# Optimization experiments

Measured on AMD Instinct MI355X. Metric: run time of the kernel, lower is better.

The kernel has to match this reference:

```python
import jax, jax.numpy as jnp
import numpy as np

ALPHA = 0.2  # leaky_relu negative slope
NEG_INF = -9e15


def gat_layer(h_in, W, a, adj_mask):
    """One GATLayer (eval mode, dropout disabled).
    h_in: [N, F_in], W: [F_in, F_out], a: [2*F_out, 1], adj_mask: [N, N] bool.
    Equivalent to the torch repeat/cat construction: e_ij = leaky_relu(a1.h_i + a2.h_j).
    """
    h = h_in @ W                          # [N, F_out]
    F_out = W.shape[1]
    a1 = a[:F_out, 0]                     # [F_out]
    a2 = a[F_out:, 0]                     # [F_out]
    f1 = h @ a1                           # [N]
    f2 = h @ a2                           # [N]
    e = jax.nn.leaky_relu(f1[:, None] + f2[None, :], negative_slope=ALPHA)  # [N, N]
    e = jnp.where(adj_mask, e, NEG_INF)
    attn = jax.nn.softmax(e, axis=-1)     # rows sum to 1
    return jax.nn.elu(attn @ h)           # [N, F_out]


def setup_inputs() -> dict:
    key = jax.random.key(0)
    ks = jax.random.split(key, 6)
    N, F_in, F_hid, F_out, H = 8192, 29, 8, 2, 4
    x = jax.random.normal(ks[0], (N, F_in), dtype=jnp.float32)
    adj = jax.random.randint(ks[1], (N, N), 0, 2, dtype=jnp.int32)
    # xavier_uniform with gain=1.414
    def xavier(k, shape, gain=1.414):
        fan_in, fan_out = shape[0], shape[1]
        bound = gain * np.sqrt(6.0 / (fan_in + fan_out))
        return jax.random.uniform(k, shape, jnp.float32, -bound, bound)
    W_heads = jnp.stack([xavier(k, (F_in, F_hid)) for k in jax.random.split(ks[2], H)])   # [H, 29, 8]
    a_heads = jnp.stack([xavier(k, (2 * F_hid, 1)) for k in jax.random.split(ks[3], H)])  # [H, 16, 1]
    W_out = xavier(ks[4], (F_hid * H, F_out))   # [32, 2]
    a_out = xavier(ks[5], (2 * F_out, 1))       # [4, 1]
    return {"x": x, "adj": adj, "W_heads": W_heads, "a_heads": a_heads,
            "W_out": W_out, "a_out": a_out}


def reference(x, adj, W_heads, a_heads, W_out, a_out):
    adj_mask = adj > 0
    heads = jax.vmap(lambda W, a: gat_layer(x, W, a, adj_mask))(W_heads, a_heads)  # [H, N, 8]
    hcat = jnp.concatenate(list(heads), axis=1)   # [N, H*8] (same order as torch cat over heads)
    out = gat_layer(hcat, W_out, a_out, adj_mask)  # [N, 2]
    return jax.nn.log_softmax(out, axis=1)
```

## Files before the change

kernel.cpp:

```cpp
#include <hip/hip_runtime.h>
#include <math.h>

#define N 8192
#define NW 128
#define FIN 29
#define FH 8
#define NH 4
#define ALPHA 0.2f
#define LOG2E 1.4426950408889634f

typedef unsigned long long ull;

__device__ inline unsigned bf16rn(float f) {
    unsigned u = __float_as_uint(f);
    return (u + 0x7fffu + ((u >> 16) & 1u)) >> 16;
}
__device__ inline float2 bfpair(unsigned u) {
    return make_float2(__uint_as_float(u << 16), __uint_as_float(u & 0xffff0000u));
}
__device__ inline unsigned fenc(float x) {
    unsigned u = __float_as_uint(x);
    return (u & 0x80000000u) ? ~u : (u | 0x80000000u);
}
__device__ inline float fdec(unsigned e) {
    return __uint_as_float((e & 0x80000000u) ? (e & 0x7fffffffu) : ~e);
}
__device__ inline float selmask(float w, ull mw) {
    unsigned lo = __builtin_amdgcn_readfirstlane((unsigned)mw);
    unsigned hi = __builtin_amdgcn_readfirstlane((unsigned)(mw >> 32));
    ull smw = ((ull)hi << 32) | lo;
    float r;
    asm("v_cndmask_b32 %0, 0, %1, %2" : "=v"(r) : "v"(w), "s"(smw));
    return r;
}

__global__ void k0_pack(const int* __restrict__ adj, ull* __restrict__ mask,
                        unsigned* __restrict__ amax) {
    int row = blockIdx.x;
    int tid = threadIdx.x;
    int lane = tid & 63;
    int wave = tid >> 6;
    if (row == 0 && tid < 8) amax[tid] = 0u;
    const int* rp = adj + (size_t)row * N;
#pragma unroll 8
    for (int i = 0; i < 32; i++) {
        int a = rp[i * 256 + tid];
        ull b = __ballot(a > 0);
        if (lane == 0) mask[(size_t)row * NW + i * 4 + wave] = b;
    }
}

__global__ __launch_bounds__(64) void k1_feat(
    const float* __restrict__ x, const float* __restrict__ Wh,
    const float* __restrict__ ah,
    float4* __restrict__ tup1, uint4* __restrict__ hpk,
    float* __restrict__ f1a, unsigned* __restrict__ amax) {
    __shared__ float sW[NH * FIN * FH];
    __shared__ float sa[NH * 2 * FH];
    int tid = threadIdx.x;
    for (int i = tid; i < NH * FIN * FH; i += 64) sW[i] = Wh[i];
    for (int i = tid; i < NH * 2 * FH; i += 64) sa[i] = ah[i];
    __syncthreads();
    int node = blockIdx.x * 64 + tid;
    float xr[FIN];
#pragma unroll
    for (int f = 0; f < FIN; f++) xr[f] = x[node * FIN + f];
    float f2v[NH];
#pragma unroll
    for (int h = 0; h < NH; h++) {
        float hv[FH];
#pragma unroll
        for (int k = 0; k < FH; k++) {
            float s = 0.f;
#pragma unroll
            for (int f = 0; f < FIN; f++) s += xr[f] * sW[(h * FIN + f) * FH + k];
            hv[k] = s;
        }
        float f1 = 0.f, f2 = 0.f;
#pragma unroll
        for (int k = 0; k < FH; k++) {
            f1 += hv[k] * sa[h * 16 + k];
            f2 += hv[k] * sa[h * 16 + 8 + k];
        }
        float f2s = f2 * LOG2E;
        f2v[h] = f2s;
        tup1[h * N + node] = make_float4(f2s,
                                         __builtin_amdgcn_exp2f(f2s),
                                         __builtin_amdgcn_exp2f(ALPHA * f2s), 0.f);
        f1a[node * 4 + h] = f1 * LOG2E;
        uint4 p;
        p.x = (bf16rn(hv[1]) << 16) | bf16rn(hv[0]);
        p.y = (bf16rn(hv[3]) << 16) | bf16rn(hv[2]);
        p.z = (bf16rn(hv[5]) << 16) | bf16rn(hv[4]);
        p.w = (bf16rn(hv[7]) << 16) | bf16rn(hv[6]);
        hpk[h * N + node] = p;
    }
#pragma unroll
    for (int h = 0; h < NH; h++) {
        float v = f2v[h];
        for (int off = 32; off > 0; off >>= 1) v = fmaxf(v, __shfl_xor(v, off, 64));
        if (tid == 0) atomicMax(&amax[h], fenc(v));
    }
}

#define TJ 512
#define JS1 2
__global__ __launch_bounds__(512) void k3_attn1(
    const ull* __restrict__ mask, const float4* __restrict__ tup1,
    const uint4* __restrict__ hpk, const float* __restrict__ f1a,
    const unsigned* __restrict__ amax, float* __restrict__ part1) {
    __shared__ float4 tT[TJ];
    __shared__ uint4 tH[TJ];
    int tid = threadIdx.x;
    int lane = tid & 63;
    int wave = tid >> 6;
    int h = blockIdx.x & 3;
    int js = (blockIdx.x >> 2) & (JS1 - 1);
    int rowblk = blockIdx.x >> 3;
    int r0 = rowblk * 32 + wave * 4;
    const int JR = N / JS1;
    int jbase = js * JR;

    float mf = fdec(amax[h]);
    float f1r[4], C1[4], C2[4];
#pragma unroll
    for (int r = 0; r < 4; r++) {
        float f1 = f1a[(r0 + r) * 4 + h];
        float v = f1 + mf, m = fmaxf(v, ALPHA * v);
        f1r[r] = f1;
        C1[r] = __builtin_amdgcn_exp2f(f1 - m);
        C2[r] = __builtin_amdgcn_exp2f(ALPHA * f1 - m);
    }
    float2 acc[4][4];
    float dsum[4];
#pragma unroll
    for (int r = 0; r < 4; r++) {
        dsum[r] = 0.f;
#pragma unroll
        for (int k = 0; k < 4; k++) acc[r][k] = make_float2(0.f, 0.f);
    }
    const ull* mr[4];
#pragma unroll
    for (int r = 0; r < 4; r++) mr[r] = mask + (size_t)(r0 + r) * NW;

    for (int t = 0; t < JR / TJ; t++) {
        __syncthreads();
        int gb = jbase + t * TJ + tid;
        tT[tid] = tup1[h * N + gb];
        tH[tid] = hpk[h * N + gb];
        __syncthreads();
        int wb = (jbase >> 6) + t * (TJ / 64);
#pragma unroll
        for (int s = 0; s < TJ / 64; s++) {
            ull mw[4];
#pragma unroll
            for (int r = 0; r < 4; r++) mw[r] = mr[r][wb + s];
            int jl = s * 64 + lane;
            float4 tq = tT[jl];
            uint4 hq = tH[jl];
            float2 hv01 = bfpair(hq.x);
            float2 hv23 = bfpair(hq.y);
            float2 hv45 = bfpair(hq.z);
            float2 hv67 = bfpair(hq.w);
#pragma unroll
            for (int r = 0; r < 4; r++) {
                float sg = f1r[r] + tq.x;
                float E = (sg >= 0.f) ? tq.y : tq.z;
                float C = (sg >= 0.f) ? C1[r] : C2[r];
                float w = selmask(C * E, mw[r]);
                acc[r][0].x = fmaf(w, hv01.x, acc[r][0].x);
                acc[r][0].y = fmaf(w, hv01.y, acc[r][0].y);
                acc[r][1].x = fmaf(w, hv23.x, acc[r][1].x);
                acc[r][1].y = fmaf(w, hv23.y, acc[r][1].y);
                acc[r][2].x = fmaf(w, hv45.x, acc[r][2].x);
                acc[r][2].y = fmaf(w, hv45.y, acc[r][2].y);
                acc[r][3].x = fmaf(w, hv67.x, acc[r][3].x);
                acc[r][3].y = fmaf(w, hv67.y, acc[r][3].y);
                dsum[r] += w;
            }
        }
    }
#pragma unroll
    for (int r = 0; r < 4; r++) {
#pragma unroll
        for (int k = 0; k < 4; k++) {
            for (int off = 32; off > 0; off >>= 1) {
                acc[r][k].x += __shfl_xor(acc[r][k].x, off, 64);
                acc[r][k].y += __shfl_xor(acc[r][k].y, off, 64);
            }
        }
        for (int off = 32; off > 0; off >>= 1)
            dsum[r] += __shfl_xor(dsum[r], off, 64);
    }
    if (lane == 0) {
#pragma unroll
        for (int r = 0; r < 4; r++) {
            int row = r0 + r;
#pragma unroll
            for (int k = 0; k < 4; k++) {
                part1[(js * 36 + h * 9 + 2 * k + 0) * N + row] = acc[r][k].x;
                part1[(js * 36 + h * 9 + 2 * k + 1) * N + row] = acc[r][k].y;
            }
            part1[(js * 36 + h * 9 + 8) * N + row] = dsum[r];
        }
    }
}

__global__ void k3b_final(const float* __restrict__ part1, const float* __restrict__ Wo,
                          const float* __restrict__ ao,
                          float4* __restrict__ rec2, float* __restrict__ f1b,
                          unsigned* __restrict__ amax) {
    __shared__ float sW[64];
    __shared__ float sa[4];
    int tid = threadIdx.x;
    if (tid < 64) sW[tid] = Wo[tid];
    if (tid < 4) sa[tid] = ao[tid];
    __syncthreads();
    int row = blockIdx.x * 256 + tid;
    float hv[32];
#pragma unroll
    for (int h = 0; h < NH; h++) {
        float s[9];
#pragma unroll
        for (int c = 0; c < 9; c++)
            s[c] = part1[(h * 9 + c) * N + row] + part1[(36 + h * 9 + c) * N + row];
        float inv = 1.f / s[8];
#pragma unroll
        for (int k = 0; k < FH; k++) {
            float o = s[k] * inv;
            hv[h * 8 + k] = (o > 0.f) ? o : expm1f(o);
        }
    }
    float h0 = 0.f, h1 = 0.f;
#pragma unroll
    for (int i = 0; i < 32; i++) {
        h0 = fmaf(hv[i], sW[i * 2 + 0], h0);
        h1 = fmaf(hv[i], sW[i * 2 + 1], h1);
    }
    float f1 = (h0 * sa[0] + h1 * sa[1]) * LOG2E;
    float f2 = (h0 * sa[2] + h1 * sa[3]) * LOG2E;
    rec2[row] = make_float4(f2, h0, h1, 0.f);
    f1b[row] = f1;
    float vmax = f2;
    for (int off = 32; off > 0; off >>= 1) vmax = fmaxf(vmax, __shfl_xor(vmax, off, 64));
    if ((tid & 63) == 0) atomicMax(&amax[4], fenc(vmax));
}

__global__ __launch_bounds__(256) void k6_attn2(
    const ull* __restrict__ mask, const float4* __restrict__ rec2,
    const float* __restrict__ f1b, const unsigned* __restrict__ amax,
    float* __restrict__ out) {
    int tid = threadIdx.x;
    int lane = tid & 63;
    int wave = tid >> 6;
    int rbase = blockIdx.x * 16 + wave * 4;

    float mb = fdec(amax[4]);
    float f1m[4], f1q[4];
#pragma unroll
    for (int i = 0; i < 4; i++) {
        float f1 = f1b[rbase + i];
        float v = f1 + mb, m = fmaxf(v, ALPHA * v);
        f1m[i] = f1 - m; f1q[i] = ALPHA * f1 - m;
    }
    float a0[4] = {0.f, 0.f, 0.f, 0.f};
    float a1[4] = {0.f, 0.f, 0.f, 0.f};
    float dd[4] = {0.f, 0.f, 0.f, 0.f};
    const ull* mr[4];
#pragma unroll
    for (int i = 0; i < 4; i++) mr[i] = mask + (size_t)(rbase + i) * NW;

#pragma unroll 4
    for (int s = 0; s < N / 64; s++) {
        float4 q = rec2[s * 64 + lane];
        float p = ALPHA * q.x;
#pragma unroll
        for (int i = 0; i < 4; i++) {
            ull mw = mr[i][s];
            float w = __builtin_amdgcn_exp2f(fmaxf(f1m[i] + q.x, p + f1q[i]));
            w = selmask(w, mw);
            a0[i] = fmaf(w, q.y, a0[i]);
            a1[i] = fmaf(w, q.z, a1[i]);
            dd[i] += w;
        }
    }
#pragma unroll
    for (int i = 0; i < 4; i++) {
        for (int off = 32; off > 0; off >>= 1) {
            a0[i] += __shfl_xor(a0[i], off, 64);
            a1[i] += __shfl_xor(a1[i], off, 64);
            dd[i] += __shfl_xor(dd[i], off, 64);
        }
    }
    if (lane == 0) {
#pragma unroll
        for (int i = 0; i < 4; i++) {
            float inv = 1.f / dd[i];
            float e0 = a0[i] * inv, e1 = a1[i] * inv;
            e0 = (e0 > 0.f) ? e0 : expm1f(e0);
            e1 = (e1 > 0.f) ? e1 : expm1f(e1);
            float mx = fmaxf(e0, e1);
            float lse = mx + logf(expf(e0 - mx) + expf(e1 - mx));
            ((float2*)out)[rbase + i] = make_float2(e0 - lse, e1 - lse);
        }
    }
}

extern "C" void kernel_launch(void* const* d_in, const int* in_sizes, int n_in,
                              void* d_out, int out_size, void* d_ws, size_t ws_size,
                              hipStream_t stream) {
    const float* x   = (const float*)d_in[0];
    const int*   adj = (const int*)d_in[1];
    const float* Wh  = (const float*)d_in[2];
    const float* ah  = (const float*)d_in[3];
    const float* Wo  = (const float*)d_in[4];
    const float* ao  = (const float*)d_in[5];
    float* out = (float*)d_out;
    float* ws = (float*)d_ws;

    ull*      mask  = (ull*)ws;
    float4*   tup1  = (float4*)(ws + 2097152);
    uint4*    hpk   = (uint4*)(ws + 2228224);
    float*    f1a   = ws + 2359296;
    float*    part1 = ws + 2392064;
    float4*   rec2  = (float4*)(ws + 2981888);
    float*    f1b   = ws + 3014656;
    unsigned* amax  = (unsigned*)(ws + 3022848);

    k0_pack<<<N, 256, 0, stream>>>(adj, mask, amax);
    k1_feat<<<N / 64, 64, 0, stream>>>(x, Wh, ah, tup1, hpk, f1a, amax);
    k3_attn1<<<(N / 32) * JS1 * NH, 512, 0, stream>>>(mask, tup1, hpk, f1a, amax, part1);
    k3b_final<<<N / 256, 256, 0, stream>>>(part1, Wo, ao, rec2, f1b, amax);
    k6_attn2<<<N / 16, 256, 0, stream>>>(mask, rec2, f1b, amax, out);
}
```

Baseline: 626.2 us.

## Use packed FMA, scalar mask loads, and precomputed exponentials in attention kernels

The first attention kernel now accumulates with v_pk_fma_f32 on two-wide float vectors, makes the mask row pointers wave-uniform so mask words can be fetched with scalar loads, and doubles the shared-memory tile to 1024 columns. The second attention kernel drops the per-element exp2 in favour of the factorised C*E trick, with per-column exp2 values computed once in k3b_final, and uses packed FMA for its two accumulators. The aim is to cut VALU instruction count and transcendental work in the inner loops. In exchange the second layer reads an extra float2 buffer, and the larger tile doubles shared memory per block, which may lower occupancy.

```diff
diff --git a/kernel.cpp b/kernel.cpp
--- a/kernel.cpp
+++ b/kernel.cpp
@@ -10,13 +10,17 @@
 #define LOG2E 1.4426950408889634f
 
 typedef unsigned long long ull;
+typedef float v2f __attribute__((ext_vector_type(2)));
 
 __device__ inline unsigned bf16rn(float f) {
     unsigned u = __float_as_uint(f);
     return (u + 0x7fffu + ((u >> 16) & 1u)) >> 16;
 }
-__device__ inline float2 bfpair(unsigned u) {
-    return make_float2(__uint_as_float(u << 16), __uint_as_float(u & 0xffff0000u));
+__device__ inline v2f bfpairv(unsigned u) {
+    v2f r;
+    r.x = __uint_as_float(u << 16);
+    r.y = __uint_as_float(u & 0xffff0000u);
+    return r;
 }
 __device__ inline unsigned fenc(float x) {
     unsigned u = __float_as_uint(x);
@@ -24,6 +28,11 @@
 }
 __device__ inline float fdec(unsigned e) {
     return __uint_as_float((e & 0x80000000u) ? (e & 0x7fffffffu) : ~e);
+}
+__device__ inline const ull* uniform_ptr(const ull* p) {
+    unsigned lo = __builtin_amdgcn_readfirstlane((unsigned)(size_t)p);
+    unsigned hi = __builtin_amdgcn_readfirstlane((unsigned)((size_t)p >> 32));
+    return (const ull*)(((size_t)hi << 32) | lo);
 }
 __device__ inline float selmask(float w, ull mw) {
     unsigned lo = __builtin_amdgcn_readfirstlane((unsigned)mw);
@@ -32,6 +41,9 @@
     float r;
     asm("v_cndmask_b32 %0, 0, %1, %2" : "=v"(r) : "v"(w), "s"(smw));
     return r;
+}
+__device__ inline void pk_fma(v2f& acc, v2f a, v2f b) {
+    asm("v_pk_fma_f32 %0, %1, %2, %0" : "+v"(acc) : "v"(a), "v"(b));
 }
 
 __global__ void k0_pack(const int* __restrict__ adj, ull* __restrict__ mask,
@@ -103,7 +115,7 @@
     }
 }
 
-#define TJ 512
+#define TJ 1024
 #define JS1 2
 __global__ __launch_bounds__(512) void k3_attn1(
     const ull* __restrict__ mask, const float4* __restrict__ tup1,
@@ -131,51 +143,53 @@
         C1[r] = __builtin_amdgcn_exp2f(f1 - m);
         C2[r] = __builtin_amdgcn_exp2f(ALPHA * f1 - m);
     }
-    float2 acc[4][4];
+    v2f acc[4][4];
     float dsum[4];
 #pragma unroll
     for (int r = 0; r < 4; r++) {
         dsum[r] = 0.f;
 #pragma unroll
-        for (int k = 0; k < 4; k++) acc[r][k] = make_float2(0.f, 0.f);
-    }
-    const ull* mr[4];
-#pragma unroll
-    for (int r = 0; r < 4; r++) mr[r] = mask + (size_t)(r0 + r) * NW;
+        for (int k = 0; k < 4; k++) { acc[r][k].x = 0.f; acc[r][k].y = 0.f; }
+    }
 
     for (int t = 0; t < JR / TJ; t++) {
         __syncthreads();
-        int gb = jbase + t * TJ + tid;
-        tT[tid] = tup1[h * N + gb];
-        tH[tid] = hpk[h * N + gb];
+#pragma unroll
+        for (int i = 0; i < TJ / 512; i++) {
+            int idx = tid + i * 512;
+            int gb = jbase + t * TJ + idx;
+            tT[idx] = tup1[h * N + gb];
+            tH[idx] = hpk[h * N + gb];
+        }
         __syncthreads();
         int wb = (jbase >> 6) + t * (TJ / 64);
+        const ull* mrs[4];
+#pragma unroll
+        for (int r = 0; r < 4; r++)
+            mrs[r] = uniform_ptr(mask + (size_t)(r0 + r) * NW + wb);
 #pragma unroll
         for (int s = 0; s < TJ / 64; s++) {
             ull mw[4];
 #pragma unroll
-            for (int r = 0; r < 4; r++) mw[r] = mr[r][wb + s];
+            for (int r = 0; r < 4; r++) mw[r] = mrs[r][s];
             int jl = s * 64 + lane;
             float4 tq = tT[jl];
             uint4 hq = tH[jl];
-            float2 hv01 = bfpair(hq.x);
-            float2 hv23 = bfpair(hq.y);
-            float2 hv45 = bfpair(hq.z);
-            float2 hv67 = bfpair(hq.w);
+            v2f hv01 = bfpairv(hq.x);
+            v2f hv23 = bfpairv(hq.y);
+            v2f hv45 = bfpairv(hq.z);
+            v2f hv67 = bfpairv(hq.w);
 #pragma unroll
             for (int r = 0; r < 4; r++) {
                 float sg = f1r[r] + tq.x;
                 float E = (sg >= 0.f) ? tq.y : tq.z;
                 float C = (sg >= 0.f) ? C1[r] : C2[r];
                 float w = selmask(C * E, mw[r]);
-                acc[r][0].x = fmaf(w, hv01.x, acc[r][0].x);
-                acc[r][0].y = fmaf(w, hv01.y, acc[r][0].y);
-                acc[r][1].x = fmaf(w, hv23.x, acc[r][1].x);
-                acc[r][1].y = fmaf(w, hv23.y, acc[r][1].y);
-                acc[r][2].x = fmaf(w, hv45.x, acc[r][2].x);
-                acc[r][2].y = fmaf(w, hv45.y, acc[r][2].y);
-                acc[r][3].x = fmaf(w, hv67.x, acc[r][3].x);
-                acc[r][3].y = fmaf(w, hv67.y, acc[r][3].y);
+                v2f w2 = {w, w};
+                pk_fma(acc[r][0], w2, hv01);
+                pk_fma(acc[r][1], w2, hv23);
+                pk_fma(acc[r][2], w2, hv45);
+                pk_fma(acc[r][3], w2, hv67);
                 dsum[r] += w;
             }
         }
@@ -208,8 +222,8 @@
 
 __global__ void k3b_final(const float* __restrict__ part1, const float* __restrict__ Wo,
                           const float* __restrict__ ao,
-                          float4* __restrict__ rec2, float* __restrict__ f1b,
-                          unsigned* __restrict__ amax) {
+                          float4* __restrict__ tup2, float2* __restrict__ h2p,
+                          float* __restrict__ f1b, unsigned* __restrict__ amax) {
     __shared__ float sW[64];
     __shared__ float sa[4];
     int tid = threadIdx.x;
@@ -239,7 +253,10 @@
     }
     float f1 = (h0 * sa[0] + h1 * sa[1]) * LOG2E;
     float f2 = (h0 * sa[2] + h1 * sa[3]) * LOG2E;
-    rec2[row] = make_float4(f2, h0, h1, 0.f);
+    tup2[row] = make_float4(f2,
+                            __builtin_amdgcn_exp2f(f2),
+                            __builtin_amdgcn_exp2f(ALPHA * f2), 0.f);
+    h2p[row] = make_float2(h0, h1);
     f1b[row] = f1;
     float vmax = f2;
     for (int off = 32; off > 0; off >>= 1) vmax = fmaxf(vmax, __shfl_xor(vmax, off, 64));
@@ -247,48 +264,55 @@
 }
 
 __global__ __launch_bounds__(256) void k6_attn2(
-    const ull* __restrict__ mask, const float4* __restrict__ rec2,
-    const float* __restrict__ f1b, const unsigned* __restrict__ amax,
-    float* __restrict__ out) {
+    const ull* __restrict__ mask, const float4* __restrict__ tup2,
+    const float2* __restrict__ h2p, const float* __restrict__ f1b,
+    const unsigned* __restrict__ amax, float* __restrict__ out) {
     int tid = threadIdx.x;
     int lane = tid & 63;
     int wave = tid >> 6;
     int rbase = blockIdx.x * 16 + wave * 4;
 
     float mb = fdec(amax[4]);
-    float f1m[4], f1q[4];
+    float f1r[4], C1[4], C2[4];
 #pragma unroll
     for (int i = 0; i < 4; i++) {
         float f1 = f1b[rbase + i];
         float v = f1 + mb, m = fmaxf(v, ALPHA * v);
-        f1m[i] = f1 - m; f1q[i] = ALPHA * f1 - m;
-    }
-    float a0[4] = {0.f, 0.f, 0.f, 0.f};
-    float a1[4] = {0.f, 0.f, 0.f, 0.f};
-    float dd[4] = {0.f, 0.f, 0.f, 0.f};
-    const ull* mr[4];
-#pragma unroll
-    for (int i = 0; i < 4; i++) mr[i] = mask + (size_t)(rbase + i) * NW;
+        f1r[i] = f1;
+        C1[i] = __builtin_amdgcn_exp2f(f1 - m);
+        C2[i] = __builtin_amdgcn_exp2f(ALPHA * f1 - m);
+    }
+    v2f a01[4];
+    float dd[4];
+#pragma unroll
+    for (int i = 0; i < 4; i++) { a01[i].x = 0.f; a01[i].y = 0.f; dd[i] = 0.f; }
+    const ull* mrs[4];
+#pragma unroll
+    for (int i = 0; i < 4; i++)
+        mrs[i] = uniform_ptr(mask + (size_t)(rbase + i) * NW);
 
 #pragma unroll 4
     for (int s = 0; s < N / 64; s++) {
-        float4 q = rec2[s * 64 + lane];
-        float p = ALPHA * q.x;
+        float4 tq = tup2[s * 64 + lane];
+        float2 hp = h2p[s * 64 + lane];
+        v2f hv = {hp.x, hp.y};
 #pragma unroll
         for (int i = 0; i < 4; i++) {
-            ull mw = mr[i][s];
-            float w = __builtin_amdgcn_exp2f(fmaxf(f1m[i] + q.x, p + f1q[i]));
-            w = selmask(w, mw);
-            a0[i] = fmaf(w, q.y, a0[i]);
-            a1[i] = fmaf(w, q.z, a1[i]);
+            ull mw = mrs[i][s];
+            float sg = f1r[i] + tq.x;
+            float E = (sg >= 0.f) ? tq.y : tq.z;
+            float C = (sg >= 0.f) ? C1[i] : C2[i];
+            float w = selmask(C * E, mw);
+            v2f w2 = {w, w};
+            pk_fma(a01[i], w2, hv);
             dd[i] += w;
         }
     }
 #pragma unroll
     for (int i = 0; i < 4; i++) {
         for (int off = 32; off > 0; off >>= 1) {
-            a0[i] += __shfl_xor(a0[i], off, 64);
-            a1[i] += __shfl_xor(a1[i], off, 64);
+            a01[i].x += __shfl_xor(a01[i].x, off, 64);
+            a01[i].y += __shfl_xor(a01[i].y, off, 64);
             dd[i] += __shfl_xor(dd[i], off, 64);
         }
     }
@@ -296,7 +320,7 @@
 #pragma unroll
         for (int i = 0; i < 4; i++) {
             float inv = 1.f / dd[i];
-            float e0 = a0[i] * inv, e1 = a1[i] * inv;
+            float e0 = a01[i].x * inv, e1 = a01[i].y * inv;
             e0 = (e0 > 0.f) ? e0 : expm1f(e0);
             e1 = (e1 > 0.f) ? e1 : expm1f(e1);
             float mx = fmaxf(e0, e1);
@@ -323,13 +347,14 @@
     uint4*    hpk   = (uint4*)(ws + 2228224);
     float*    f1a   = ws + 2359296;
     float*    part1 = ws + 2392064;
-    float4*   rec2  = (float4*)(ws + 2981888);
-    float*    f1b   = ws + 3014656;
-    unsigned* amax  = (unsigned*)(ws + 3022848);
+    float4*   tup2  = (float4*)(ws + 2981888);
+    float2*   h2p   = (float2*)(ws + 3014656);
+    float*    f1b   = ws + 3031040;
+    unsigned* amax  = (unsigned*)(ws + 3039232);
 
     k0_pack<<<N, 256, 0, stream>>>(adj, mask, amax);
     k1_feat<<<N / 64, 64, 0, stream>>>(x, Wh, ah, tup1, hpk, f1a, amax);
     k3_attn1<<<(N / 32) * JS1 * NH, 512, 0, stream>>>(mask, tup1, hpk, f1a, amax, part1);
-    k3b_final<<<N / 256, 256, 0, stream>>>(part1, Wo, ao, rec2, f1b, amax);
-    k6_attn2<<<N / 16, 256, 0, stream>>>(mask, rec2, f1b, amax, out);
-}
+    k3b_final<<<N / 256, 256, 0, stream>>>(part1, Wo, ao, tup2, h2p, f1b, amax);
+    k6_attn2<<<N / 16, 256, 0, stream>>>(mask, tup2, h2p, f1b, amax, out);
+}
```

Result: slower. 655.9 us (+4.7%).
